# Kernel tuning notes

Measured on AMD Instinct MI355X. Metric: run time of the kernel, lower is better.

Reference implementation:

```python
import jax, jax.numpy as jnp
import numpy as np
import math

N_HEADS = 32
N_REP = 4
N_KV = N_HEADS // N_REP
HEAD_DIM = 128
MAX_SEQ = 4096
BATCH = 8
Q_LEN = 1


def setup_inputs() -> dict:
    key = jax.random.key(0)
    ks = jax.random.split(key, 7)
    input_pos = jax.random.randint(ks[0], (Q_LEN,), 0, MAX_SEQ, dtype=jnp.int32)
    q = jax.random.normal(ks[1], (N_HEADS, BATCH, Q_LEN, HEAD_DIM), dtype=jnp.float32)
    k = jax.random.normal(ks[2], (N_KV, BATCH, Q_LEN, HEAD_DIM), dtype=jnp.float32)
    v = jax.random.normal(ks[3], (N_KV, BATCH, Q_LEN, HEAD_DIM), dtype=jnp.float32)
    k_cache = jax.random.normal(ks[4], (N_KV, BATCH, MAX_SEQ, HEAD_DIM), dtype=jnp.float32)
    v_cache = jax.random.normal(ks[5], (N_KV, BATCH, MAX_SEQ, HEAD_DIM), dtype=jnp.float32)
    mask = jax.random.normal(ks[6], (MAX_SEQ, MAX_SEQ), dtype=jnp.float32)
    return {"input_pos": input_pos, "q": q, "k": k, "v": v,
            "k_cache": k_cache, "v_cache": v_cache, "mask": mask}


def reference(input_pos, q, k, v, k_cache, v_cache, mask):
    # KV cache update (index_put_ at positions input_pos along seq axis)
    kc = k_cache.at[:, :, input_pos, :].set(k)   # [G, B, S, D]
    vc = v_cache.at[:, :, input_pos, :].set(v)   # [G, B, S, D]
    scale = 1.0 / math.sqrt(HEAD_DIM)
    # group query heads by kv head: head i uses kv group i // n_rep
    qg = q.reshape(N_KV, N_REP, BATCH, Q_LEN, HEAD_DIM)
    scores = jnp.einsum('grbqd,gbsd->grbqs', qg, kc) * scale
    scores = scores + mask[input_pos]            # [Q, S] broadcast
    probs = jax.nn.softmax(scores, axis=-1)
    out = jnp.einsum('grbqs,gbsd->grbqd', probs, vc)  # [G, R, B, Q, D]
    # torch.cat over heads (i = g*n_rep + r) on last dim -> [B, Q, H*D]
    out = out.transpose(2, 3, 0, 1, 4).reshape(BATCH, Q_LEN, N_HEADS * HEAD_DIM)
    return out
```

## Files before the change

kernel.cpp:

```cpp
#include <hip/hip_runtime.h>
#include <math.h>

#define NKV    8
#define NREP   4
#define NH     32
#define BATCH  8
#define D      128
#define SEQ    4096
#define CHUNKS 32
#define CS     128
#define PSTRIDE 130

__global__ __launch_bounds__(256, 4) void attn_partial(
    const int*   __restrict__ input_pos,
    const float* __restrict__ q,
    const float* __restrict__ knew,
    const float* __restrict__ vnew,
    const float* __restrict__ kcache,
    const float* __restrict__ vcache,
    const float* __restrict__ mask,
    float*       __restrict__ ws)
{
    const int pair = blockIdx.x;
    const int c    = blockIdx.y;
    const int g    = pair >> 3;
    const int b    = pair & 7;
    const int t    = threadIdx.x;
    const int w    = t >> 6;
    const int lane = t & 63;
    const int p4   = lane >> 4;
    const int l16  = lane & 15;
    const int pos  = input_pos[0];

    __shared__ float sc[NREP][CS];
    __shared__ float ml[NREP][2];
    __shared__ float opart[4][NREP][D];

    const float  scale  = 0.08838834764831845f;
    const size_t kvbase = (size_t)(g * BATCH + b) * SEQ * D;
    const float* kbase  = kcache + kvbase;
    const float* vbase  = vcache + kvbase;
    const float* mrow   = mask + (size_t)pos * SEQ;
    const float* knewr  = knew + (size_t)(g * BATCH + b) * D;
    const float* vnewr  = vnew + (size_t)(g * BATCH + b) * D;
    const int    s0     = c * CS;
    const int    rowbase = w * 32;

    float4 qv[NREP][2];
    #pragma unroll
    for (int r = 0; r < NREP; ++r) {
        const float4* qr = (const float4*)(q + ((size_t)(g * NREP + r) * BATCH + b) * D
                                           + l16 * 8);
        qv[r][0] = qr[0];
        qv[r][1] = qr[1];
    }

    float4 kb[8][2];
    #pragma unroll
    for (int i = 0; i < 8; ++i) {
        const int s = s0 + rowbase + i * 4 + p4;
        const float* krow = (s == pos) ? knewr : (kbase + (size_t)s * D);
        const float4* k4  = (const float4*)(krow + l16 * 8);
        kb[i][0] = k4[0];
        kb[i][1] = k4[1];
    }

    #pragma unroll
    for (int i = 0; i < 8; ++i) {
        const int sl = rowbase + i * 4 + p4;
        float acc[NREP];
        #pragma unroll
        for (int r = 0; r < NREP; ++r) {
            float a;
            a = kb[i][0].x * qv[r][0].x;
            a = fmaf(kb[i][0].y, qv[r][0].y, a);
            a = fmaf(kb[i][0].z, qv[r][0].z, a);
            a = fmaf(kb[i][0].w, qv[r][0].w, a);
            a = fmaf(kb[i][1].x, qv[r][1].x, a);
            a = fmaf(kb[i][1].y, qv[r][1].y, a);
            a = fmaf(kb[i][1].z, qv[r][1].z, a);
            a = fmaf(kb[i][1].w, qv[r][1].w, a);
            acc[r] = a;
        }
        #pragma unroll
        for (int off = 1; off < 16; off <<= 1) {
            #pragma unroll
            for (int r = 0; r < NREP; ++r)
                acc[r] += __shfl_xor(acc[r], off);
        }
        if (l16 == 0) {
            const float mval = mrow[s0 + sl];
            #pragma unroll
            for (int r = 0; r < NREP; ++r)
                sc[r][sl] = acc[r] * scale + mval;
        }
    }
    __syncthreads();

    const int half = lane >> 5;
    const int l32  = lane & 31;
    float4 vv[16];
    #pragma unroll
    for (int it = 0; it < 16; ++it) {
        const int s = s0 + rowbase + it * 2 + half;
        const float* vrow = (s == pos) ? vnewr : (vbase + (size_t)s * D);
        vv[it] = *(const float4*)(vrow + l32 * 4);
    }

    {
        const int r = w;
        float v0 = sc[r][lane];
        float v1 = sc[r][lane + 64];
        float m  = fmaxf(v0, v1);
        #pragma unroll
        for (int off = 1; off < 64; off <<= 1)
            m = fmaxf(m, __shfl_xor(m, off));
        float e0 = __expf(v0 - m);
        float e1 = __expf(v1 - m);
        sc[r][lane]      = e0;
        sc[r][lane + 64] = e1;
        float l = e0 + e1;
        #pragma unroll
        for (int off = 1; off < 64; off <<= 1)
            l += __shfl_xor(l, off);
        if (lane == 0) { ml[r][0] = m; ml[r][1] = l; }
    }
    __syncthreads();

    float4 oacc[NREP];
    #pragma unroll
    for (int r = 0; r < NREP; ++r) oacc[r] = make_float4(0.f, 0.f, 0.f, 0.f);

    #pragma unroll
    for (int it = 0; it < 16; ++it) {
        const int sl = rowbase + it * 2 + half;
        const float4 v4 = vv[it];
        #pragma unroll
        for (int r = 0; r < NREP; ++r) {
            const float pr = sc[r][sl];
            oacc[r].x = fmaf(pr, v4.x, oacc[r].x);
            oacc[r].y = fmaf(pr, v4.y, oacc[r].y);
            oacc[r].z = fmaf(pr, v4.z, oacc[r].z);
            oacc[r].w = fmaf(pr, v4.w, oacc[r].w);
        }
    }
    #pragma unroll
    for (int r = 0; r < NREP; ++r) {
        oacc[r].x += __shfl_xor(oacc[r].x, 32);
        oacc[r].y += __shfl_xor(oacc[r].y, 32);
        oacc[r].z += __shfl_xor(oacc[r].z, 32);
        oacc[r].w += __shfl_xor(oacc[r].w, 32);
    }
    if (half == 0) {
        #pragma unroll
        for (int r = 0; r < NREP; ++r)
            *(float4*)&opart[w][r][l32 * 4] = oacc[r];
    }
    __syncthreads();

    #pragma unroll
    for (int ii = 0; ii < 2; ++ii) {
        int idx = t + ii * 256;
        int r   = idx >> 7;
        int d   = idx & 127;
        float sum = opart[0][r][d] + opart[1][r][d]
                  + opart[2][r][d] + opart[3][r][d];
        size_t base = (((size_t)pair * CHUNKS + c) * NREP + r) * PSTRIDE;
        ws[base + d] = sum;
        if (d == 0) { ws[base + 128] = ml[r][0]; ws[base + 129] = ml[r][1]; }
    }
}

__global__ __launch_bounds__(128) void attn_reduce(
    const float* __restrict__ ws, float* __restrict__ out)
{
    const int idx  = blockIdx.x;
    const int pair = idx >> 2;
    const int r    = idx & 3;
    const int g    = pair >> 3;
    const int b    = pair & 7;
    const int d    = threadIdx.x;

    float mv[CHUNKS], lv[CHUNKS];
    float M = -INFINITY;
    #pragma unroll
    for (int c = 0; c < CHUNKS; ++c) {
        size_t base = (((size_t)pair * CHUNKS + c) * NREP + r) * PSTRIDE;
        float2 t = *(const float2*)&ws[base + 128];
        mv[c] = t.x; lv[c] = t.y;
        M = fmaxf(M, t.x);
    }
    float acc = 0.f, L = 0.f;
    #pragma unroll
    for (int c = 0; c < CHUNKS; ++c) {
        size_t base = (((size_t)pair * CHUNKS + c) * NREP + r) * PSTRIDE;
        float wgt = __expf(mv[c] - M);
        acc += ws[base + d] * wgt;
        L   += lv[c] * wgt;
    }
    int h = g * NREP + r;
    out[(size_t)b * (NH * D) + h * D + d] = acc / L;
}

__global__ __launch_bounds__(256) void attn_full(
    const int*   __restrict__ input_pos,
    const float* __restrict__ q,
    const float* __restrict__ knew,
    const float* __restrict__ vnew,
    const float* __restrict__ kcache,
    const float* __restrict__ vcache,
    const float* __restrict__ mask,
    float*       __restrict__ out)
{
    const int idx = blockIdx.x;
    const int h   = idx >> 3;
    const int b   = idx & 7;
    const int g   = h >> 2;
    const int t   = threadIdx.x;
    const int wave = t >> 6, lane = t & 63, half = lane >> 5, l32 = lane & 31;
    const int pos = input_pos[0];

    __shared__ float sc[SEQ];
    __shared__ float wred[4];
    __shared__ float oacc[2][D];

    const size_t kvbase = (size_t)(g * BATCH + b) * SEQ * D;
    const float* kbase  = kcache + kvbase;
    const float* vbase  = vcache + kvbase;
    const float* mrow   = mask + (size_t)pos * SEQ;
    const float* knewr  = knew + (size_t)(g * BATCH + b) * D;
    const float* vnewr  = vnew + (size_t)(g * BATCH + b) * D;
    const float  scale  = 0.08838834764831845f;

    float4 qv = ((const float4*)(q + (size_t)(h * BATCH + b) * D))[l32];

    for (int p = 0; p < SEQ / 8; ++p) {
        int s = p * 8 + wave * 2 + half;
        const float4* krow = (s == pos) ? (const float4*)knewr
                                        : (const float4*)(kbase + (size_t)s * D);
        float4 kv = krow[l32];
        float acc = qv.x * kv.x + qv.y * kv.y + qv.z * kv.z + qv.w * kv.w;
        #pragma unroll
        for (int off = 1; off < 32; off <<= 1)
            acc += __shfl_xor(acc, off);
        if (l32 == 0) sc[s] = acc * scale + mrow[s];
    }
    __syncthreads();

    float m = -INFINITY;
    for (int s = t; s < SEQ; s += 256) m = fmaxf(m, sc[s]);
    #pragma unroll
    for (int off = 1; off < 64; off <<= 1) m = fmaxf(m, __shfl_xor(m, off));
    if (lane == 0) wred[wave] = m;
    __syncthreads();
    m = fmaxf(fmaxf(wred[0], wred[1]), fmaxf(wred[2], wred[3]));
    __syncthreads();

    float l = 0.f;
    for (int s = t; s < SEQ; s += 256) { float e = __expf(sc[s] - m); sc[s] = e; l += e; }
    #pragma unroll
    for (int off = 1; off < 64; off <<= 1) l += __shfl_xor(l, off);
    __syncthreads();
    if (lane == 0) wred[wave] = l;
    __syncthreads();
    float L = wred[0] + wred[1] + wred[2] + wred[3];

    {
        int hf = t >> 7, d = t & 127;
        float acc = 0.f;
        for (int s = hf * (SEQ / 2); s < (hf + 1) * (SEQ / 2); ++s) {
            const float* vrow = (s == pos) ? vnewr : (vbase + (size_t)s * D);
            acc += sc[s] * vrow[d];
        }
        oacc[hf][d] = acc;
    }
    __syncthreads();
    if (t < D) out[(size_t)b * (NH * D) + h * D + t] = (oacc[0][t] + oacc[1][t]) / L;
}

extern "C" void kernel_launch(void* const* d_in, const int* in_sizes, int n_in,
                              void* d_out, int out_size, void* d_ws, size_t ws_size,
                              hipStream_t stream) {
    const int*   input_pos = (const int*)  d_in[0];
    const float* q         = (const float*)d_in[1];
    const float* k         = (const float*)d_in[2];
    const float* v         = (const float*)d_in[3];
    const float* kcache    = (const float*)d_in[4];
    const float* vcache    = (const float*)d_in[5];
    const float* mask      = (const float*)d_in[6];
    float* out = (float*)d_out;

    const size_t need = (size_t)64 * CHUNKS * NREP * PSTRIDE * sizeof(float);
    if (ws_size >= need) {
        dim3 g1(64, CHUNKS);
        attn_partial<<<g1, 256, 0, stream>>>(input_pos, q, k, v, kcache, vcache, mask,
                                             (float*)d_ws);
        attn_reduce<<<256, 128, 0, stream>>>((const float*)d_ws, out);
    } else {
        attn_full<<<256, 256, 0, stream>>>(input_pos, q, k, v, kcache, vcache, mask, out);
    }
}
```

Baseline: 51.85 us.

## Stage K and V tiles into LDS via global_load_lds in half-chunks

K and V rows are no longer loaded into registers. They are copied straight from global memory into a shared 64-row LDS buffer with the direct global-to-LDS load builtin, in two halves per chunk, and the same buffer is reused for the output partials. The aim is to cut VGPR pressure and the register round-trip of the cache loads. In exchange, each chunk's loads are split into serialized stage/compute phases separated by extra barriers, so fewer loads are in flight. This could hurt a kernel that already streams near memory bandwidth.

```diff
diff --git a/kernel.cpp b/kernel.cpp
--- a/kernel.cpp
+++ b/kernel.cpp
@@ -9,7 +9,15 @@
 #define SEQ    4096
 #define CHUNKS 32
 #define CS     128
+#define HROWS  64
 #define PSTRIDE 130
+
+__device__ __forceinline__ void stage16(const float* src, float* lds_dst) {
+    __builtin_amdgcn_global_load_lds(
+        (const __attribute__((address_space(1))) void*)src,
+        (__attribute__((address_space(3))) void*)lds_dst,
+        16, 0, 0);
+}
 
 __global__ __launch_bounds__(256, 4) void attn_partial(
     const int*   __restrict__ input_pos,
@@ -30,11 +38,14 @@
     const int lane = t & 63;
     const int p4   = lane >> 4;
     const int l16  = lane & 15;
+    const int vh   = lane >> 5;
+    const int l32  = lane & 31;
     const int pos  = input_pos[0];
 
+    __shared__ __align__(16) float buf[HROWS * D];
     __shared__ float sc[NREP][CS];
     __shared__ float ml[NREP][2];
-    __shared__ float opart[4][NREP][D];
+    float (*opart)[NREP][D] = (float (*)[NREP][D])buf;
 
     const float  scale  = 0.08838834764831845f;
     const size_t kvbase = (size_t)(g * BATCH + b) * SEQ * D;
@@ -44,7 +55,6 @@
     const float* knewr  = knew + (size_t)(g * BATCH + b) * D;
     const float* vnewr  = vnew + (size_t)(g * BATCH + b) * D;
     const int    s0     = c * CS;
-    const int    rowbase = w * 32;
 
     float4 qv[NREP][2];
     #pragma unroll
@@ -55,57 +65,63 @@
         qv[r][1] = qr[1];
     }
 
-    float4 kb[8][2];
-    #pragma unroll
-    for (int i = 0; i < 8; ++i) {
-        const int s = s0 + rowbase + i * 4 + p4;
-        const float* krow = (s == pos) ? knewr : (kbase + (size_t)s * D);
-        const float4* k4  = (const float4*)(krow + l16 * 8);
-        kb[i][0] = k4[0];
-        kb[i][1] = k4[1];
-    }
-
-    #pragma unroll
-    for (int i = 0; i < 8; ++i) {
-        const int sl = rowbase + i * 4 + p4;
-        float acc[NREP];
-        #pragma unroll
-        for (int r = 0; r < NREP; ++r) {
-            float a;
-            a = kb[i][0].x * qv[r][0].x;
-            a = fmaf(kb[i][0].y, qv[r][0].y, a);
-            a = fmaf(kb[i][0].z, qv[r][0].z, a);
-            a = fmaf(kb[i][0].w, qv[r][0].w, a);
-            a = fmaf(kb[i][1].x, qv[r][1].x, a);
-            a = fmaf(kb[i][1].y, qv[r][1].y, a);
-            a = fmaf(kb[i][1].z, qv[r][1].z, a);
-            a = fmaf(kb[i][1].w, qv[r][1].w, a);
-            acc[r] = a;
+    auto stage_half = [&](const float* base, const float* newrow, int hh) {
+        #pragma unroll
+        for (int jj = 0; jj < 8; ++jj) {
+            const int j  = w * 8 + jj;
+            const int rl = 2 * j + vh;
+            const int s  = s0 + hh * HROWS + rl;
+            const float* src = ((s == pos) ? newrow : (base + (size_t)s * D)) + l32 * 4;
+            stage16(src, &buf[j * 256]);
         }
-        #pragma unroll
-        for (int off = 1; off < 16; off <<= 1) {
+    };
+
+    auto scores_half = [&](int hh) {
+        #pragma unroll
+        for (int i = 0; i < 4; ++i) {
+            const int rl = w * 16 + i * 4 + p4;
+            const int sl = hh * HROWS + rl;
+            const float4* kr = (const float4*)&buf[rl * D + l16 * 8];
+            const float4 k0 = kr[0], k1 = kr[1];
+            float acc[NREP];
             #pragma unroll
-            for (int r = 0; r < NREP; ++r)
-                acc[r] += __shfl_xor(acc[r], off);
+            for (int r = 0; r < NREP; ++r) {
+                float a;
+                a = k0.x * qv[r][0].x;
+                a = fmaf(k0.y, qv[r][0].y, a);
+                a = fmaf(k0.z, qv[r][0].z, a);
+                a = fmaf(k0.w, qv[r][0].w, a);
+                a = fmaf(k1.x, qv[r][1].x, a);
+                a = fmaf(k1.y, qv[r][1].y, a);
+                a = fmaf(k1.z, qv[r][1].z, a);
+                a = fmaf(k1.w, qv[r][1].w, a);
+                acc[r] = a;
+            }
+            #pragma unroll
+            for (int off = 1; off < 16; off <<= 1) {
+                #pragma unroll
+                for (int r = 0; r < NREP; ++r)
+                    acc[r] += __shfl_xor(acc[r], off);
+            }
+            if (l16 == 0) {
+                const float mval = mrow[s0 + sl];
+                #pragma unroll
+                for (int r = 0; r < NREP; ++r)
+                    sc[r][sl] = acc[r] * scale + mval;
+            }
         }
-        if (l16 == 0) {
-            const float mval = mrow[s0 + sl];
-            #pragma unroll
-            for (int r = 0; r < NREP; ++r)
-                sc[r][sl] = acc[r] * scale + mval;
-        }
-    }
-    __syncthreads();
-
-    const int half = lane >> 5;
-    const int l32  = lane & 31;
-    float4 vv[16];
-    #pragma unroll
-    for (int it = 0; it < 16; ++it) {
-        const int s = s0 + rowbase + it * 2 + half;
-        const float* vrow = (s == pos) ? vnewr : (vbase + (size_t)s * D);
-        vv[it] = *(const float4*)(vrow + l32 * 4);
-    }
+    };
+
+    stage_half(kbase, knewr, 0);
+    __syncthreads();
+    scores_half(0);
+    __syncthreads();
+    stage_half(kbase, knewr, 1);
+    __syncthreads();
+    scores_half(1);
+    __syncthreads();
+
+    stage_half(vbase, vnewr, 0);
 
     {
         const int r = w;
@@ -131,19 +147,29 @@
     #pragma unroll
     for (int r = 0; r < NREP; ++r) oacc[r] = make_float4(0.f, 0.f, 0.f, 0.f);
 
-    #pragma unroll
-    for (int it = 0; it < 16; ++it) {
-        const int sl = rowbase + it * 2 + half;
-        const float4 v4 = vv[it];
-        #pragma unroll
-        for (int r = 0; r < NREP; ++r) {
-            const float pr = sc[r][sl];
-            oacc[r].x = fmaf(pr, v4.x, oacc[r].x);
-            oacc[r].y = fmaf(pr, v4.y, oacc[r].y);
-            oacc[r].z = fmaf(pr, v4.z, oacc[r].z);
-            oacc[r].w = fmaf(pr, v4.w, oacc[r].w);
+    auto pv_half = [&](int hh) {
+        #pragma unroll
+        for (int it = 0; it < 8; ++it) {
+            const int rl = w * 16 + it * 2 + vh;
+            const int sl = hh * HROWS + rl;
+            const float4 v4 = *(const float4*)&buf[rl * D + l32 * 4];
+            #pragma unroll
+            for (int r = 0; r < NREP; ++r) {
+                const float pr = sc[r][sl];
+                oacc[r].x = fmaf(pr, v4.x, oacc[r].x);
+                oacc[r].y = fmaf(pr, v4.y, oacc[r].y);
+                oacc[r].z = fmaf(pr, v4.z, oacc[r].z);
+                oacc[r].w = fmaf(pr, v4.w, oacc[r].w);
+            }
         }
-    }
+    };
+
+    pv_half(0);
+    __syncthreads();
+    stage_half(vbase, vnewr, 1);
+    __syncthreads();
+    pv_half(1);
+
     #pragma unroll
     for (int r = 0; r < NREP; ++r) {
         oacc[r].x += __shfl_xor(oacc[r].x, 32);
@@ -151,7 +177,8 @@
         oacc[r].z += __shfl_xor(oacc[r].z, 32);
         oacc[r].w += __shfl_xor(oacc[r].w, 32);
     }
-    if (half == 0) {
+    __syncthreads();
+    if (vh == 0) {
         #pragma unroll
         for (int r = 0; r < NREP; ++r)
             *(float4*)&opart[w][r][l32 * 4] = oacc[r];
```

After: 52.75 us. Within noise of the previous version (+1.7%).

## Split KV into 64-row chunks with 128-thread blocks and vectorized softmax

Applied to the files above, without the earlier changes.

Adds a new partial kernel that processes 64-row chunks with two warps per block, giving 4096 blocks instead of 2048. It stores the four per-head scores as a float4 and does the softmax for all four heads in one wave. K and V loads are interleaved with compute instead of being prefetched into large register arrays. The reduce kernel takes the chunk count at runtime, which doubles its work and drops the unrolled register caching. The chunk-128 kernel stays as a fallback for smaller workspaces.

```diff
diff --git a/kernel.cpp b/kernel.cpp
--- a/kernel.cpp
+++ b/kernel.cpp
@@ -7,11 +7,175 @@
 #define BATCH  8
 #define D      128
 #define SEQ    4096
-#define CHUNKS 32
-#define CS     128
 #define PSTRIDE 130
 
-__global__ __launch_bounds__(256, 4) void attn_partial(
+__global__ __launch_bounds__(128, 6) void attn_partial64(
+    const int*   __restrict__ input_pos,
+    const float* __restrict__ q,
+    const float* __restrict__ knew,
+    const float* __restrict__ vnew,
+    const float* __restrict__ kcache,
+    const float* __restrict__ vcache,
+    const float* __restrict__ mask,
+    float*       __restrict__ ws)
+{
+    const int pair = blockIdx.x;
+    const int c    = blockIdx.y;
+    const int g    = pair >> 3;
+    const int b    = pair & 7;
+    const int t    = threadIdx.x;
+    const int w    = t >> 6;
+    const int lane = t & 63;
+    const int p4   = lane >> 4;
+    const int l16  = lane & 15;
+    const int vh   = lane >> 5;
+    const int l32  = lane & 31;
+    const int pos  = input_pos[0];
+
+    __shared__ float4 sc4[64];
+    __shared__ float  opart[2][NREP][D];
+
+    const float  scale  = 0.08838834764831845f;
+    const size_t kvbase = (size_t)(g * BATCH + b) * SEQ * D;
+    const float* kbase  = kcache + kvbase;
+    const float* vbase  = vcache + kvbase;
+    const float* mrow   = mask + (size_t)pos * SEQ;
+    const float* knewr  = knew + (size_t)(g * BATCH + b) * D;
+    const float* vnewr  = vnew + (size_t)(g * BATCH + b) * D;
+    const int    s0     = c * 64;
+
+    float4 qv[NREP][2];
+    #pragma unroll
+    for (int r = 0; r < NREP; ++r) {
+        const float4* qr = (const float4*)(q + ((size_t)(g * NREP + r) * BATCH + b) * D
+                                           + l16 * 8);
+        qv[r][0] = qr[0];
+        qv[r][1] = qr[1];
+    }
+
+    #pragma unroll
+    for (int i = 0; i < 8; ++i) {
+        const int rl = w * 32 + i * 4 + p4;
+        const int s  = s0 + rl;
+        const float* krow = (s == pos) ? knewr : (kbase + (size_t)s * D);
+        const float4* k4  = (const float4*)(krow + l16 * 8);
+        const float4 k0 = k4[0], k1 = k4[1];
+        float acc[NREP];
+        #pragma unroll
+        for (int r = 0; r < NREP; ++r) {
+            float a;
+            a = k0.x * qv[r][0].x;
+            a = fmaf(k0.y, qv[r][0].y, a);
+            a = fmaf(k0.z, qv[r][0].z, a);
+            a = fmaf(k0.w, qv[r][0].w, a);
+            a = fmaf(k1.x, qv[r][1].x, a);
+            a = fmaf(k1.y, qv[r][1].y, a);
+            a = fmaf(k1.z, qv[r][1].z, a);
+            a = fmaf(k1.w, qv[r][1].w, a);
+            acc[r] = a;
+        }
+        #pragma unroll
+        for (int off = 1; off < 16; off <<= 1) {
+            #pragma unroll
+            for (int r = 0; r < NREP; ++r)
+                acc[r] += __shfl_xor(acc[r], off);
+        }
+        if (l16 == 0) {
+            const float mval = mrow[s];
+            sc4[rl] = make_float4(fmaf(acc[0], scale, mval),
+                                  fmaf(acc[1], scale, mval),
+                                  fmaf(acc[2], scale, mval),
+                                  fmaf(acc[3], scale, mval));
+        }
+    }
+    __syncthreads();
+
+    float4 sv = sc4[lane];
+    float4 mm = sv;
+    #pragma unroll
+    for (int off = 1; off < 64; off <<= 1) {
+        mm.x = fmaxf(mm.x, __shfl_xor(mm.x, off));
+        mm.y = fmaxf(mm.y, __shfl_xor(mm.y, off));
+        mm.z = fmaxf(mm.z, __shfl_xor(mm.z, off));
+        mm.w = fmaxf(mm.w, __shfl_xor(mm.w, off));
+    }
+    float4 ev;
+    ev.x = __expf(sv.x - mm.x);
+    ev.y = __expf(sv.y - mm.y);
+    ev.z = __expf(sv.z - mm.z);
+    ev.w = __expf(sv.w - mm.w);
+    if (w == 0) sc4[lane] = ev;
+    float4 LL = ev;
+    #pragma unroll
+    for (int off = 1; off < 64; off <<= 1) {
+        LL.x += __shfl_xor(LL.x, off);
+        LL.y += __shfl_xor(LL.y, off);
+        LL.z += __shfl_xor(LL.z, off);
+        LL.w += __shfl_xor(LL.w, off);
+    }
+    __syncthreads();
+
+    float4 oacc[NREP];
+    #pragma unroll
+    for (int r = 0; r < NREP; ++r) oacc[r] = make_float4(0.f, 0.f, 0.f, 0.f);
+
+    #pragma unroll
+    for (int it = 0; it < 16; ++it) {
+        const int rl = w * 32 + it * 2 + vh;
+        const int s  = s0 + rl;
+        const float* vrow = (s == pos) ? vnewr : (vbase + (size_t)s * D);
+        const float4 vv  = *(const float4*)(vrow + l32 * 4);
+        const float4 pr  = sc4[rl];
+        oacc[0].x = fmaf(pr.x, vv.x, oacc[0].x);
+        oacc[0].y = fmaf(pr.x, vv.y, oacc[0].y);
+        oacc[0].z = fmaf(pr.x, vv.z, oacc[0].z);
+        oacc[0].w = fmaf(pr.x, vv.w, oacc[0].w);
+        oacc[1].x = fmaf(pr.y, vv.x, oacc[1].x);
+        oacc[1].y = fmaf(pr.y, vv.y, oacc[1].y);
+        oacc[1].z = fmaf(pr.y, vv.z, oacc[1].z);
+        oacc[1].w = fmaf(pr.y, vv.w, oacc[1].w);
+        oacc[2].x = fmaf(pr.z, vv.x, oacc[2].x);
+        oacc[2].y = fmaf(pr.z, vv.y, oacc[2].y);
+        oacc[2].z = fmaf(pr.z, vv.z, oacc[2].z);
+        oacc[2].w = fmaf(pr.z, vv.w, oacc[2].w);
+        oacc[3].x = fmaf(pr.w, vv.x, oacc[3].x);
+        oacc[3].y = fmaf(pr.w, vv.y, oacc[3].y);
+        oacc[3].z = fmaf(pr.w, vv.z, oacc[3].z);
+        oacc[3].w = fmaf(pr.w, vv.w, oacc[3].w);
+    }
+    #pragma unroll
+    for (int r = 0; r < NREP; ++r) {
+        oacc[r].x += __shfl_xor(oacc[r].x, 32);
+        oacc[r].y += __shfl_xor(oacc[r].y, 32);
+        oacc[r].z += __shfl_xor(oacc[r].z, 32);
+        oacc[r].w += __shfl_xor(oacc[r].w, 32);
+    }
+    if (vh == 0) {
+        #pragma unroll
+        for (int r = 0; r < NREP; ++r)
+            *(float4*)&opart[w][r][l32 * 4] = oacc[r];
+    }
+    __syncthreads();
+
+    #pragma unroll
+    for (int ii = 0; ii < 4; ++ii) {
+        int idx = t + ii * 128;
+        int r   = idx >> 7;
+        int d   = idx & 127;
+        float sum = opart[0][r][d] + opart[1][r][d];
+        size_t base = (((size_t)pair * 64 + c) * NREP + r) * PSTRIDE;
+        ws[base + d] = sum;
+    }
+    if (t == 0) {
+        size_t base = (((size_t)pair * 64 + c) * NREP) * PSTRIDE;
+        ws[base + 128] = mm.x;               ws[base + 129] = LL.x;
+        ws[base + PSTRIDE + 128] = mm.y;     ws[base + PSTRIDE + 129] = LL.y;
+        ws[base + 2 * PSTRIDE + 128] = mm.z; ws[base + 2 * PSTRIDE + 129] = LL.z;
+        ws[base + 3 * PSTRIDE + 128] = mm.w; ws[base + 3 * PSTRIDE + 129] = LL.w;
+    }
+}
+
+__global__ __launch_bounds__(256, 4) void attn_partial128(
     const int*   __restrict__ input_pos,
     const float* __restrict__ q,
     const float* __restrict__ knew,
@@ -32,7 +196,7 @@
     const int l16  = lane & 15;
     const int pos  = input_pos[0];
 
-    __shared__ float sc[NREP][CS];
+    __shared__ float sc[NREP][128];
     __shared__ float ml[NREP][2];
     __shared__ float opart[4][NREP][D];
 
@@ -43,7 +207,7 @@
     const float* mrow   = mask + (size_t)pos * SEQ;
     const float* knewr  = knew + (size_t)(g * BATCH + b) * D;
     const float* vnewr  = vnew + (size_t)(g * BATCH + b) * D;
-    const int    s0     = c * CS;
+    const int    s0     = c * 128;
     const int    rowbase = w * 32;
 
     float4 qv[NREP][2];
@@ -55,31 +219,25 @@
         qv[r][1] = qr[1];
     }
 
-    float4 kb[8][2];
     #pragma unroll
     for (int i = 0; i < 8; ++i) {
-        const int s = s0 + rowbase + i * 4 + p4;
+        const int sl = rowbase + i * 4 + p4;
+        const int s  = s0 + sl;
         const float* krow = (s == pos) ? knewr : (kbase + (size_t)s * D);
         const float4* k4  = (const float4*)(krow + l16 * 8);
-        kb[i][0] = k4[0];
-        kb[i][1] = k4[1];
-    }
-
-    #pragma unroll
-    for (int i = 0; i < 8; ++i) {
-        const int sl = rowbase + i * 4 + p4;
+        const float4 k0 = k4[0], k1 = k4[1];
         float acc[NREP];
         #pragma unroll
         for (int r = 0; r < NREP; ++r) {
             float a;
-            a = kb[i][0].x * qv[r][0].x;
-            a = fmaf(kb[i][0].y, qv[r][0].y, a);
-            a = fmaf(kb[i][0].z, qv[r][0].z, a);
-            a = fmaf(kb[i][0].w, qv[r][0].w, a);
-            a = fmaf(kb[i][1].x, qv[r][1].x, a);
-            a = fmaf(kb[i][1].y, qv[r][1].y, a);
-            a = fmaf(kb[i][1].z, qv[r][1].z, a);
-            a = fmaf(kb[i][1].w, qv[r][1].w, a);
+            a = k0.x * qv[r][0].x;
+            a = fmaf(k0.y, qv[r][0].y, a);
+            a = fmaf(k0.z, qv[r][0].z, a);
+            a = fmaf(k0.w, qv[r][0].w, a);
+            a = fmaf(k1.x, qv[r][1].x, a);
+            a = fmaf(k1.y, qv[r][1].y, a);
+            a = fmaf(k1.z, qv[r][1].z, a);
+            a = fmaf(k1.w, qv[r][1].w, a);
             acc[r] = a;
         }
         #pragma unroll
@@ -89,23 +247,13 @@
                 acc[r] += __shfl_xor(acc[r], off);
         }
         if (l16 == 0) {
-            const float mval = mrow[s0 + sl];
+            const float mval = mrow[s];
             #pragma unroll
             for (int r = 0; r < NREP; ++r)
-                sc[r][sl] = acc[r] * scale + mval;
-        }
-    }
-    __syncthreads();
-
-    const int half = lane >> 5;
-    const int l32  = lane & 31;
-    float4 vv[16];
-    #pragma unroll
-    for (int it = 0; it < 16; ++it) {
-        const int s = s0 + rowbase + it * 2 + half;
-        const float* vrow = (s == pos) ? vnewr : (vbase + (size_t)s * D);
-        vv[it] = *(const float4*)(vrow + l32 * 4);
-    }
+                sc[r][sl] = fmaf(acc[r], scale, mval);
+        }
+    }
+    __syncthreads();
 
     {
         const int r = w;
@@ -127,6 +275,8 @@
     }
     __syncthreads();
 
+    const int half = lane >> 5;
+    const int l32  = lane & 31;
     float4 oacc[NREP];
     #pragma unroll
     for (int r = 0; r < NREP; ++r) oacc[r] = make_float4(0.f, 0.f, 0.f, 0.f);
@@ -134,7 +284,9 @@
     #pragma unroll
     for (int it = 0; it < 16; ++it) {
         const int sl = rowbase + it * 2 + half;
-        const float4 v4 = vv[it];
+        const int s  = s0 + sl;
+        const float* vrow = (s == pos) ? vnewr : (vbase + (size_t)s * D);
+        const float4 v4 = *(const float4*)(vrow + l32 * 4);
         #pragma unroll
         for (int r = 0; r < NREP; ++r) {
             const float pr = sc[r][sl];
@@ -165,14 +317,14 @@
         int d   = idx & 127;
         float sum = opart[0][r][d] + opart[1][r][d]
                   + opart[2][r][d] + opart[3][r][d];
-        size_t base = (((size_t)pair * CHUNKS + c) * NREP + r) * PSTRIDE;
+        size_t base = (((size_t)pair * 32 + c) * NREP + r) * PSTRIDE;
         ws[base + d] = sum;
         if (d == 0) { ws[base + 128] = ml[r][0]; ws[base + 129] = ml[r][1]; }
     }
 }
 
 __global__ __launch_bounds__(128) void attn_reduce(
-    const float* __restrict__ ws, float* __restrict__ out)
+    const float* __restrict__ ws, float* __restrict__ out, int nchunks)
 {
     const int idx  = blockIdx.x;
     const int pair = idx >> 2;
@@ -181,22 +333,18 @@
     const int b    = pair & 7;
     const int d    = threadIdx.x;
 
-    float mv[CHUNKS], lv[CHUNKS];
+    const size_t base0 = (((size_t)pair * nchunks) * NREP + r) * PSTRIDE;
+    const size_t cstep = (size_t)NREP * PSTRIDE;
+
     float M = -INFINITY;
-    #pragma unroll
-    for (int c = 0; c < CHUNKS; ++c) {
-        size_t base = (((size_t)pair * CHUNKS + c) * NREP + r) * PSTRIDE;
-        float2 t = *(const float2*)&ws[base + 128];
-        mv[c] = t.x; lv[c] = t.y;
-        M = fmaxf(M, t.x);
-    }
+    for (int c = 0; c < nchunks; ++c)
+        M = fmaxf(M, ws[base0 + c * cstep + 128]);
     float acc = 0.f, L = 0.f;
-    #pragma unroll
-    for (int c = 0; c < CHUNKS; ++c) {
-        size_t base = (((size_t)pair * CHUNKS + c) * NREP + r) * PSTRIDE;
-        float wgt = __expf(mv[c] - M);
+    for (int c = 0; c < nchunks; ++c) {
+        size_t base = base0 + c * cstep;
+        float wgt = __expf(ws[base + 128] - M);
         acc += ws[base + d] * wgt;
-        L   += lv[c] * wgt;
+        L   += ws[base + 129] * wgt;
     }
     int h = g * NREP + r;
     out[(size_t)b * (NH * D) + h * D + d] = acc / L;
@@ -290,12 +438,18 @@
     const float* mask      = (const float*)d_in[6];
     float* out = (float*)d_out;
 
-    const size_t need = (size_t)64 * CHUNKS * NREP * PSTRIDE * sizeof(float);
-    if (ws_size >= need) {
-        dim3 g1(64, CHUNKS);
-        attn_partial<<<g1, 256, 0, stream>>>(input_pos, q, k, v, kcache, vcache, mask,
-                                             (float*)d_ws);
-        attn_reduce<<<256, 128, 0, stream>>>((const float*)d_ws, out);
+    const size_t need64 = (size_t)64 * 64 * NREP * PSTRIDE * sizeof(float);
+    const size_t need32 = (size_t)64 * 32 * NREP * PSTRIDE * sizeof(float);
+    if (ws_size >= need64) {
+        dim3 g1(64, 64);
+        attn_partial64<<<g1, 128, 0, stream>>>(input_pos, q, k, v, kcache, vcache, mask,
+                                               (float*)d_ws);
+        attn_reduce<<<256, 128, 0, stream>>>((const float*)d_ws, out, 64);
+    } else if (ws_size >= need32) {
+        dim3 g1(64, 32);
+        attn_partial128<<<g1, 256, 0, stream>>>(input_pos, q, k, v, kcache, vcache, mask,
+                                                (float*)d_ws);
+        attn_reduce<<<256, 128, 0, stream>>>((const float*)d_ws, out, 32);
     } else {
         attn_full<<<256, 256, 0, stream>>>(input_pos, q, k, v, kcache, vcache, mask, out);
     }
```

Result: slower. 89.00 us (+71.7%).

## Double sequence chunk size and stream K/V loads inline instead of prefetching

Applied to the files above, without the earlier changes.

Doubles the per-block sequence chunk to 256 rows, which halves the number of chunks and the partial results the combine stage has to merge. K rows are now loaded inside the dot-product loop rather than staged into a register array first. V rows are loaded inside the PV loop after softmax, so they no longer overlap with the softmax phase. This cuts the grid in half and reduces combine work, but it lowers parallelism and gives up the latency hiding that the early V prefetch provided.

```diff
diff --git a/kernel.cpp b/kernel.cpp
--- a/kernel.cpp
+++ b/kernel.cpp
@@ -7,8 +7,8 @@
 #define BATCH  8
 #define D      128
 #define SEQ    4096
-#define CHUNKS 32
-#define CS     128
+#define CHUNKS 16
+#define CS     256
 #define PSTRIDE 130
 
 __global__ __launch_bounds__(256, 4) void attn_partial(
@@ -30,6 +30,8 @@
     const int lane = t & 63;
     const int p4   = lane >> 4;
     const int l16  = lane & 15;
+    const int half = lane >> 5;
+    const int l32  = lane & 31;
     const int pos  = input_pos[0];
 
     __shared__ float sc[NREP][CS];
@@ -44,7 +46,7 @@
     const float* knewr  = knew + (size_t)(g * BATCH + b) * D;
     const float* vnewr  = vnew + (size_t)(g * BATCH + b) * D;
     const int    s0     = c * CS;
-    const int    rowbase = w * 32;
+    const int    rowbase = w * 64;
 
     float4 qv[NREP][2];
     #pragma unroll
@@ -55,31 +57,25 @@
         qv[r][1] = qr[1];
     }
 
-    float4 kb[8][2];
-    #pragma unroll
-    for (int i = 0; i < 8; ++i) {
-        const int s = s0 + rowbase + i * 4 + p4;
+    #pragma unroll
+    for (int i = 0; i < 16; ++i) {
+        const int sl = rowbase + i * 4 + p4;
+        const int s  = s0 + sl;
         const float* krow = (s == pos) ? knewr : (kbase + (size_t)s * D);
         const float4* k4  = (const float4*)(krow + l16 * 8);
-        kb[i][0] = k4[0];
-        kb[i][1] = k4[1];
-    }
-
-    #pragma unroll
-    for (int i = 0; i < 8; ++i) {
-        const int sl = rowbase + i * 4 + p4;
+        const float4 k0 = k4[0], k1 = k4[1];
         float acc[NREP];
         #pragma unroll
         for (int r = 0; r < NREP; ++r) {
             float a;
-            a = kb[i][0].x * qv[r][0].x;
-            a = fmaf(kb[i][0].y, qv[r][0].y, a);
-            a = fmaf(kb[i][0].z, qv[r][0].z, a);
-            a = fmaf(kb[i][0].w, qv[r][0].w, a);
-            a = fmaf(kb[i][1].x, qv[r][1].x, a);
-            a = fmaf(kb[i][1].y, qv[r][1].y, a);
-            a = fmaf(kb[i][1].z, qv[r][1].z, a);
-            a = fmaf(kb[i][1].w, qv[r][1].w, a);
+            a = k0.x * qv[r][0].x;
+            a = fmaf(k0.y, qv[r][0].y, a);
+            a = fmaf(k0.z, qv[r][0].z, a);
+            a = fmaf(k0.w, qv[r][0].w, a);
+            a = fmaf(k1.x, qv[r][1].x, a);
+            a = fmaf(k1.y, qv[r][1].y, a);
+            a = fmaf(k1.z, qv[r][1].z, a);
+            a = fmaf(k1.w, qv[r][1].w, a);
             acc[r] = a;
         }
         #pragma unroll
@@ -89,37 +85,33 @@
                 acc[r] += __shfl_xor(acc[r], off);
         }
         if (l16 == 0) {
-            const float mval = mrow[s0 + sl];
+            const float mval = mrow[s];
             #pragma unroll
             for (int r = 0; r < NREP; ++r)
-                sc[r][sl] = acc[r] * scale + mval;
-        }
-    }
-    __syncthreads();
-
-    const int half = lane >> 5;
-    const int l32  = lane & 31;
-    float4 vv[16];
-    #pragma unroll
-    for (int it = 0; it < 16; ++it) {
-        const int s = s0 + rowbase + it * 2 + half;
-        const float* vrow = (s == pos) ? vnewr : (vbase + (size_t)s * D);
-        vv[it] = *(const float4*)(vrow + l32 * 4);
-    }
+                sc[r][sl] = fmaf(acc[r], scale, mval);
+        }
+    }
+    __syncthreads();
 
     {
         const int r = w;
         float v0 = sc[r][lane];
         float v1 = sc[r][lane + 64];
-        float m  = fmaxf(v0, v1);
+        float v2 = sc[r][lane + 128];
+        float v3 = sc[r][lane + 192];
+        float m  = fmaxf(fmaxf(v0, v1), fmaxf(v2, v3));
         #pragma unroll
         for (int off = 1; off < 64; off <<= 1)
             m = fmaxf(m, __shfl_xor(m, off));
         float e0 = __expf(v0 - m);
         float e1 = __expf(v1 - m);
-        sc[r][lane]      = e0;
-        sc[r][lane + 64] = e1;
-        float l = e0 + e1;
+        float e2 = __expf(v2 - m);
+        float e3 = __expf(v3 - m);
+        sc[r][lane]       = e0;
+        sc[r][lane + 64]  = e1;
+        sc[r][lane + 128] = e2;
+        sc[r][lane + 192] = e3;
+        float l = (e0 + e1) + (e2 + e3);
         #pragma unroll
         for (int off = 1; off < 64; off <<= 1)
             l += __shfl_xor(l, off);
@@ -132,9 +124,11 @@
     for (int r = 0; r < NREP; ++r) oacc[r] = make_float4(0.f, 0.f, 0.f, 0.f);
 
     #pragma unroll
-    for (int it = 0; it < 16; ++it) {
+    for (int it = 0; it < 32; ++it) {
         const int sl = rowbase + it * 2 + half;
-        const float4 v4 = vv[it];
+        const int s  = s0 + sl;
+        const float* vrow = (s == pos) ? vnewr : (vbase + (size_t)s * D);
+        const float4 v4 = *(const float4*)(vrow + l32 * 4);
         #pragma unroll
         for (int r = 0; r < NREP; ++r) {
             const float pr = sc[r][sl];
```

Result: slower. 54.56 us (+5.2%).
